# Kernel optimization log

Measured on AMD Instinct MI355X. Metric: run time of the kernel, lower is better.

Reference implementation:

```python
import jax, jax.numpy as jnp
import numpy as np

N, E, IN, H, C = 20000, 320000, 512, 4, 64
HC = H * C
EPS_BN = 1e-5


def setup_inputs() -> dict:
    key = jax.random.key(0)
    ks = jax.random.split(key, 12)
    p = lambda k, shape, s=0.05: jax.random.normal(k, shape, dtype=jnp.float32) * s
    z = lambda n: jnp.zeros((n,), jnp.float32)
    o = lambda n: jnp.ones((n,), jnp.float32)
    return {
        "x": jax.random.normal(ks[0], (N, IN), dtype=jnp.float32),
        "edge_index": jax.random.randint(ks[1], (2, E), 0, N),
        "Wl0": p(ks[2], (IN, HC)), "Wr0": p(ks[3], (IN, HC)),
        "att0": p(ks[4], (H, C)), "b0": z(HC),
        "g0": o(HC), "be0": z(HC), "m0": z(HC), "v0": o(HC),
        "Wl1": p(ks[5], (HC, HC)), "Wr1": p(ks[6], (HC, HC)),
        "att1": p(ks[7], (H, C)), "b1": z(HC),
        "g1": o(HC), "be1": z(HC), "m1": z(HC), "v1": o(HC),
        "Wl2": p(ks[8], (HC, 2)), "Wr2": p(ks[9], (HC, 2)),
        "att2": p(ks[10], (1, 2)), "b2": z(2),
    }


def gatv2_conv(x, Wl, Wr, att, b, ei, concat):
    # GATv2: e_ij = att . LeakyReLU(Wl x_j + Wr x_i); softmax over in-edges of i
    n = x.shape[0]
    h, c = att.shape
    xl = (x @ Wl).reshape(n, h, c)  # source/message transform
    xr = (x @ Wr).reshape(n, h, c)  # target transform
    src, dst = ei[0], ei[1]
    m = xl[src] + xr[dst]                                   # [E,H,C] edge gather
    e = jnp.sum(jax.nn.leaky_relu(m, 0.2) * att, axis=-1)   # [E,H]
    emax = jax.ops.segment_max(e, dst, num_segments=n)      # segment softmax
    emax = jnp.where(jnp.isfinite(emax), emax, 0.0)
    ex = jnp.exp(e - emax[dst])
    denom = jax.ops.segment_sum(ex, dst, num_segments=n)
    alpha = ex / (denom[dst] + 1e-16)                       # [E,H]
    out = jax.ops.segment_sum(alpha[:, :, None] * xl[src], dst, num_segments=n)
    out = out.reshape(n, h * c) if concat else out.mean(axis=1)
    return out + b


def bn_eval(x, g, be, m, v):
    return (x - m) * (g * jax.lax.rsqrt(v + EPS_BN)) + be


def reference(x, edge_index, Wl0, Wr0, att0, b0, g0, be0, m0, v0,
              Wl1, Wr1, att1, b1, g1, be1, m1, v1, Wl2, Wr2, att2, b2):
    loops = jnp.arange(N)
    ei = jnp.concatenate([edge_index, jnp.stack([loops, loops])], axis=1)
    h = gatv2_conv(x, Wl0, Wr0, att0, b0, ei, True)
    h = jax.nn.elu(bn_eval(h, g0, be0, m0, v0))
    h = gatv2_conv(h, Wl1, Wr1, att1, b1, ei, True)
    h = jax.nn.elu(bn_eval(h, g1, be1, m1, v1))
    out = gatv2_conv(h, Wl2, Wr2, att2, b2, ei, False)
    return jax.nn.log_softmax(out, axis=1)
```

## Files before the change

kernel.cpp:

```cpp
#include <hip/hip_runtime.h>
#include <math.h>

#define NN 20000
#define MP 20096
#define EE 320000
#define ET (EE + NN)
#define HC 256
#define EPS_BN 1e-5f

#define PB_CX 5000
#define PB_W0 1024
#define PB_W1 512
#define PB_HIST 1329
#define PB_TOTAL (PB_CX + PB_W0 + PB_W1 + PB_HIST)

typedef __bf16 bf16x8 __attribute__((ext_vector_type(8)));
typedef float f32x4 __attribute__((ext_vector_type(4)));

__device__ __forceinline__ float4 ld4(const float* p) { return *reinterpret_cast<const float4*>(p); }
__device__ __forceinline__ float lrelu(float x) { return fmaxf(x, 0.f) + 0.2f * fminf(x, 0.f); }

__device__ __forceinline__ unsigned short f2b(float f) {
  unsigned int u = __float_as_uint(f);
  u = (u + 0x7fffu + ((u >> 16) & 1u)) >> 16;
  return (unsigned short)u;
}
__device__ __forceinline__ float b2f(unsigned short u) {
  return __uint_as_float(((unsigned int)u) << 16);
}

__device__ __forceinline__ void gld_lds16(const void* g, void* l) {
  __builtin_amdgcn_global_load_lds(
      (const __attribute__((address_space(1))) unsigned int*)g,
      (__attribute__((address_space(3))) unsigned int*)(unsigned int)(unsigned long long)l,
      16, 0, 0);
}

__global__ __launch_bounds__(256) void prep_kernel(const float* __restrict__ x,
                                                   unsigned short* __restrict__ xb,
                                                   const float* __restrict__ Wl0,
                                                   const float* __restrict__ Wr0,
                                                   unsigned short* __restrict__ Wf0,
                                                   const float* __restrict__ Wl1,
                                                   const float* __restrict__ Wr1,
                                                   unsigned short* __restrict__ Wf1,
                                                   const int* __restrict__ ei,
                                                   int* __restrict__ counts) {
  const int b = blockIdx.x;
  const int tid = threadIdx.x;
  if (b < PB_CX) {
    int i = (b * 256 + tid) * 8;
    float4 v0 = ld4(&x[i]);
    float4 v1 = ld4(&x[i + 4]);
    ushort4 o0, o1;
    o0.x = f2b(v0.x); o0.y = f2b(v0.y); o0.z = f2b(v0.z); o0.w = f2b(v0.w);
    o1.x = f2b(v1.x); o1.y = f2b(v1.y); o1.z = f2b(v1.z); o1.w = f2b(v1.w);
    *reinterpret_cast<ushort4*>(&xb[i]) = o0;
    *reinterpret_cast<ushort4*>(&xb[i + 4]) = o1;
  } else if (b < PB_CX + PB_W0) {
    int idx = (b - PB_CX) * 256 + tid;
    int n = idx >> 9, k = idx & 511;
    float v = (n < 256) ? Wl0[(size_t)k * 256 + n] : Wr0[(size_t)k * 256 + (n - 256)];
    Wf0[idx] = f2b(v);
  } else if (b < PB_CX + PB_W0 + PB_W1) {
    int idx = (b - PB_CX - PB_W0) * 256 + tid;
    int n = idx >> 8, k = idx & 255;
    float v = (n < 256) ? Wl1[(size_t)k * 256 + n] : Wr1[(size_t)k * 256 + (n - 256)];
    Wf1[idx] = f2b(v);
  } else {
    int e = (b - PB_CX - PB_W0 - PB_W1) * 256 + tid;
    if (e < ET) {
      int d = (e < EE) ? ei[EE + e] : (e - EE);
      atomicAdd(&counts[d], 1);
    }
  }
}

__global__ __launch_bounds__(256) void gemm_mfma(const unsigned short* __restrict__ A,
                                                 const unsigned short* __restrict__ Bt,
                                                 unsigned short* __restrict__ xlb,
                                                 float* __restrict__ xrf,
                                                 int M, int K) {
  __shared__ unsigned short As[128 * 32];
  __shared__ unsigned short Bs[128 * 32];
  const int wave = threadIdx.x >> 6;
  const int lane = threadIdx.x & 63;
  const int am = lane & 15;
  const int aq = lane >> 4;
  const int wr = (wave >> 1) * 64;
  const int wc = (wave & 1) * 64;
  const int row0 = blockIdx.y * 128;
  const int col0 = blockIdx.x * 128;

  f32x4 acc[4][4] = {};

  for (int kk = 0; kk < K; kk += 32) {
    __syncthreads();
#pragma unroll
    for (int c = 0; c < 2; ++c) {
      int seg = wave * 128 + c * 64 + lane;
      int r = seg >> 2, ks = (seg & 3) * 8;
      gld_lds16(A + (size_t)(row0 + r) * K + kk + ks, &As[(wave * 128 + c * 64) * 8]);
      gld_lds16(Bt + (size_t)(col0 + r) * K + kk + ks, &Bs[(wave * 128 + c * 64) * 8]);
    }
    __syncthreads();

    bf16x8 af[4], bfr[4];
#pragma unroll
    for (int i = 0; i < 4; ++i)
      af[i] = *reinterpret_cast<const bf16x8*>(&As[(wr + i * 16 + am) * 32 + aq * 8]);
#pragma unroll
    for (int j = 0; j < 4; ++j)
      bfr[j] = *reinterpret_cast<const bf16x8*>(&Bs[(wc + j * 16 + am) * 32 + aq * 8]);
#pragma unroll
    for (int i = 0; i < 4; ++i)
#pragma unroll
      for (int j = 0; j < 4; ++j)
        acc[i][j] = __builtin_amdgcn_mfma_f32_16x16x32_bf16(af[i], bfr[j], acc[i][j], 0, 0, 0);
  }

#pragma unroll
  for (int i = 0; i < 4; ++i) {
#pragma unroll
    for (int j = 0; j < 4; ++j) {
      int gcol = col0 + wc + j * 16 + am;
#pragma unroll
      for (int rr = 0; rr < 4; ++rr) {
        int grow = row0 + wr + i * 16 + aq * 4 + rr;
        if (grow < M) {
          float v = acc[i][j][rr];
          if (gcol < 256) xlb[(size_t)grow * 256 + gcol] = f2b(v);
          else            xrf[(size_t)grow * 256 + (gcol - 256)] = v;
        }
      }
    }
  }
}

__global__ __launch_bounds__(1024) void scan_kernel(int* __restrict__ cursor,
                                                    int* __restrict__ offsets) {
  __shared__ int wsum[16];
  const int tid = threadIdx.x;
  const int lane = tid & 63, wv = tid >> 6;
  const int base = tid * 20;
  int vals[20];
  int s = 0;
  if (tid < 1000) {
#pragma unroll
    for (int j = 0; j < 20; ++j) { vals[j] = cursor[base + j]; s += vals[j]; }
  }
  int ssum = s;
#pragma unroll
  for (int off = 1; off < 64; off <<= 1) {
    int t = __shfl_up(ssum, off);
    if (lane >= off) ssum += t;
  }
  if (lane == 63) wsum[wv] = ssum;
  __syncthreads();
  if (wv == 0) {
    int w = (lane < 16) ? wsum[lane] : 0;
#pragma unroll
    for (int off = 1; off < 16; off <<= 1) {
      int t = __shfl_up(w, off);
      if (lane >= off) w += t;
    }
    if (lane < 16) wsum[lane] = w;
  }
  __syncthreads();
  int excl = ssum - s + (wv > 0 ? wsum[wv - 1] : 0);
  if (tid < 1000) {
    int run = excl;
#pragma unroll
    for (int j = 0; j < 20; ++j) { offsets[base + j] = run; cursor[base + j] = run; run += vals[j]; }
  }
  if (tid == 1023) offsets[NN] = wsum[15];
}

__global__ __launch_bounds__(256) void scatter_kernel(const int* __restrict__ ei,
                                                      int* __restrict__ cursor,
                                                      int* __restrict__ srcs) {
  int e = blockIdx.x * blockDim.x + threadIdx.x;
  if (e >= ET) return;
  int s, d;
  if (e < EE) { s = ei[e]; d = ei[EE + e]; } else { s = d = e - EE; }
  int pos = atomicAdd(&cursor[d], 1);
  srcs[pos] = s;
}

__global__ __launch_bounds__(256) void gat_layer(const unsigned short* __restrict__ xlb,
                                                 const float* __restrict__ xrf,
                                                 const float* __restrict__ att,
                                                 const float* __restrict__ bias,
                                                 const float* __restrict__ gam,
                                                 const float* __restrict__ bet,
                                                 const float* __restrict__ mean,
                                                 const float* __restrict__ var,
                                                 const int* __restrict__ offsets,
                                                 const int* __restrict__ srcs,
                                                 unsigned short* __restrict__ hb) {
  const int wave = threadIdx.x >> 6;
  const int lane = threadIdx.x & 63;
  const int node = blockIdx.x * 4 + wave;
  if (node >= NN) return;

  const float4 xr4 = ld4(&xrf[(size_t)node * HC + lane * 4]);
  const float4 a4 = ld4(&att[lane * 4]);
  const int beg = offsets[node];
  const int deg = offsets[node + 1] - beg;

  float lA = 0.f, lB = 0.f;
  float4 OA = make_float4(0.f, 0.f, 0.f, 0.f);
  float4 OB = make_float4(0.f, 0.f, 0.f, 0.f);

  for (int base = 0; base < deg; base += 64) {
    const int chunk = min(64, deg - base);
    const int s_reg = srcs[beg + base + min(lane, chunk - 1)];
    const int nb = (chunk + 3) >> 2;

    ushort4 buf0[4], buf1[4], buf2[4];

#define ISSUE(r, buf)                                                              \
    {                                                                              \
      _Pragma("unroll")                                                            \
      for (int j = 0; j < 4; ++j) {                                                \
        int idx = (r) * 4 + j;                                                     \
        int sv = __shfl(s_reg, idx < chunk ? idx : 0);                             \
        buf[j] = *reinterpret_cast<const ushort4*>(&xlb[(size_t)sv * HC + lane * 4]); \
      }                                                                            \
    }

#define COMPUTE(r, buf)                                                            \
    {                                                                              \
      float e[4], xv[4][4];                                                        \
      _Pragma("unroll")                                                            \
      for (int j = 0; j < 4; ++j) {                                                \
        xv[j][0] = b2f(buf[j].x); xv[j][1] = b2f(buf[j].y);                        \
        xv[j][2] = b2f(buf[j].z); xv[j][3] = b2f(buf[j].w);                        \
        e[j] = lrelu(xv[j][0] + xr4.x) * a4.x + lrelu(xv[j][1] + xr4.y) * a4.y +   \
               lrelu(xv[j][2] + xr4.z) * a4.z + lrelu(xv[j][3] + xr4.w) * a4.w;    \
      }                                                                            \
      _Pragma("unroll")                                                            \
      for (int off = 1; off < 16; off <<= 1) {                                     \
        e[0] += __shfl_xor(e[0], off); e[1] += __shfl_xor(e[1], off);              \
        e[2] += __shfl_xor(e[2], off); e[3] += __shfl_xor(e[3], off);              \
      }                                                                            \
      float p0 = __expf(e[0]), p1 = __expf(e[1]);                                  \
      float p2 = __expf(e[2]), p3 = __expf(e[3]);                                  \
      if ((r) * 4 + 0 >= chunk) p0 = 0.f;                                          \
      if ((r) * 4 + 1 >= chunk) p1 = 0.f;                                          \
      if ((r) * 4 + 2 >= chunk) p2 = 0.f;                                          \
      if ((r) * 4 + 3 >= chunk) p3 = 0.f;                                          \
      lA += p0; lB += p1; lA += p2; lB += p3;                                      \
      OA.x += p0 * xv[0][0]; OA.y += p0 * xv[0][1];                                \
      OA.z += p0 * xv[0][2]; OA.w += p0 * xv[0][3];                                \
      OB.x += p1 * xv[1][0]; OB.y += p1 * xv[1][1];                                \
      OB.z += p1 * xv[1][2]; OB.w += p1 * xv[1][3];                                \
      OA.x += p2 * xv[2][0]; OA.y += p2 * xv[2][1];                                \
      OA.z += p2 * xv[2][2]; OA.w += p2 * xv[2][3];                                \
      OB.x += p3 * xv[3][0]; OB.y += p3 * xv[3][1];                                \
      OB.z += p3 * xv[3][2]; OB.w += p3 * xv[3][3];                                \
    }

    ISSUE(0, buf0);
    ISSUE(1, buf1);
    ISSUE(2, buf2);
    int r = 0;
    while (r < nb) {
      COMPUTE(r, buf0); if (r + 3 < nb) ISSUE(r + 3, buf0); ++r;
      if (r >= nb) break;
      COMPUTE(r, buf1); if (r + 3 < nb) ISSUE(r + 3, buf1); ++r;
      if (r >= nb) break;
      COMPUTE(r, buf2); if (r + 3 < nb) ISSUE(r + 3, buf2); ++r;
    }
#undef ISSUE
#undef COMPUTE
  }

  float inv = 1.f / (lA + lB);
  float4 O = make_float4(OA.x + OB.x, OA.y + OB.y, OA.z + OB.z, OA.w + OB.w);

  float4 b4 = ld4(&bias[lane * 4]);
  float4 g4 = ld4(&gam[lane * 4]);
  float4 e4 = ld4(&bet[lane * 4]);
  float4 m4 = ld4(&mean[lane * 4]);
  float4 v4 = ld4(&var[lane * 4]);
  float y0 = O.x * inv + b4.x, y1 = O.y * inv + b4.y;
  float y2 = O.z * inv + b4.z, y3 = O.w * inv + b4.w;
  float z0 = (y0 - m4.x) * (g4.x * rsqrtf(v4.x + EPS_BN)) + e4.x;
  float z1 = (y1 - m4.y) * (g4.y * rsqrtf(v4.y + EPS_BN)) + e4.y;
  float z2 = (y2 - m4.z) * (g4.z * rsqrtf(v4.z + EPS_BN)) + e4.z;
  float z3 = (y3 - m4.w) * (g4.w * rsqrtf(v4.w + EPS_BN)) + e4.w;
  ushort4 r4o;
  r4o.x = f2b(z0 > 0.f ? z0 : expm1f(z0));
  r4o.y = f2b(z1 > 0.f ? z1 : expm1f(z1));
  r4o.z = f2b(z2 > 0.f ? z2 : expm1f(z2));
  r4o.w = f2b(z3 > 0.f ? z3 : expm1f(z3));
  *reinterpret_cast<ushort4*>(&hb[(size_t)node * HC + lane * 4]) = r4o;
}

__global__ __launch_bounds__(256) void lin2_kernel(const unsigned short* __restrict__ hb,
                                                   const float* __restrict__ Wl,
                                                   const float* __restrict__ Wr,
                                                   float* __restrict__ xl2,
                                                   float* __restrict__ xr2) {
  const int wave = threadIdx.x >> 6;
  const int lane = threadIdx.x & 63;
  const int node = blockIdx.x * 4 + wave;
  if (node >= NN) return;
  ushort4 h4 = *reinterpret_cast<const ushort4*>(&hb[(size_t)node * HC + lane * 4]);
  float hv[4] = {b2f(h4.x), b2f(h4.y), b2f(h4.z), b2f(h4.w)};
  float l0 = 0.f, l1 = 0.f, r0 = 0.f, r1 = 0.f;
#pragma unroll
  for (int j = 0; j < 4; ++j) {
    int row = lane * 4 + j;
    l0 += hv[j] * Wl[row * 2 + 0];
    l1 += hv[j] * Wl[row * 2 + 1];
    r0 += hv[j] * Wr[row * 2 + 0];
    r1 += hv[j] * Wr[row * 2 + 1];
  }
#pragma unroll
  for (int off = 1; off < 64; off <<= 1) {
    l0 += __shfl_xor(l0, off);
    l1 += __shfl_xor(l1, off);
    r0 += __shfl_xor(r0, off);
    r1 += __shfl_xor(r1, off);
  }
  if (lane == 0) {
    xl2[node * 2 + 0] = l0; xl2[node * 2 + 1] = l1;
    xr2[node * 2 + 0] = r0; xr2[node * 2 + 1] = r1;
  }
}

__global__ __launch_bounds__(256) void gat2_out_kernel(const float* __restrict__ xl2,
                                                       const float* __restrict__ xr2,
                                                       const float* __restrict__ att2,
                                                       const float* __restrict__ b2,
                                                       const int* __restrict__ offsets,
                                                       const int* __restrict__ srcs,
                                                       float* __restrict__ out) {
  const int wave = threadIdx.x >> 6;
  const int lane = threadIdx.x & 63;
  const int node = blockIdx.x * 4 + wave;
  if (node >= NN) return;
  const float a0 = att2[0], a1 = att2[1];
  const float xr0 = xr2[node * 2 + 0], xr1 = xr2[node * 2 + 1];
  const int beg = offsets[node], end = offsets[node + 1];

  float l = 0.f, o0 = 0.f, o1 = 0.f;
  for (int i = beg + lane; i < end; i += 64) {
    int s = srcs[i];
    float x0 = xl2[s * 2 + 0], x1 = xl2[s * 2 + 1];
    float e = lrelu(x0 + xr0) * a0 + lrelu(x1 + xr1) * a1;
    float p = __expf(e);
    l += p;
    o0 += p * x0;
    o1 += p * x1;
  }
#pragma unroll
  for (int off = 1; off < 64; off <<= 1) {
    l += __shfl_xor(l, off);
    o0 += __shfl_xor(o0, off);
    o1 += __shfl_xor(o1, off);
  }
  if (lane == 0) {
    float inv = 1.f / l;
    float t0 = o0 * inv + b2[0];
    float t1 = o1 * inv + b2[1];
    float mx = fmaxf(t0, t1);
    float ls = mx + logf(__expf(t0 - mx) + __expf(t1 - mx));
    out[node * 2 + 0] = t0 - ls;
    out[node * 2 + 1] = t1 - ls;
  }
}

extern "C" void kernel_launch(void* const* d_in, const int* in_sizes, int n_in,
                              void* d_out, int out_size, void* d_ws, size_t ws_size,
                              hipStream_t stream) {
  const float* x    = (const float*)d_in[0];
  const int*   ei   = (const int*)d_in[1];
  const float* Wl0  = (const float*)d_in[2];
  const float* Wr0  = (const float*)d_in[3];
  const float* att0 = (const float*)d_in[4];
  const float* b0   = (const float*)d_in[5];
  const float* g0   = (const float*)d_in[6];
  const float* be0  = (const float*)d_in[7];
  const float* m0   = (const float*)d_in[8];
  const float* v0   = (const float*)d_in[9];
  const float* Wl1  = (const float*)d_in[10];
  const float* Wr1  = (const float*)d_in[11];
  const float* att1 = (const float*)d_in[12];
  const float* b1   = (const float*)d_in[13];
  const float* g1   = (const float*)d_in[14];
  const float* be1  = (const float*)d_in[15];
  const float* m1   = (const float*)d_in[16];
  const float* v1   = (const float*)d_in[17];
  const float* Wl2  = (const float*)d_in[18];
  const float* Wr2  = (const float*)d_in[19];
  const float* att2 = (const float*)d_in[20];
  const float* b2   = (const float*)d_in[21];

  float* xrf = (float*)d_ws;
  unsigned short* xlb = (unsigned short*)(xrf + (size_t)NN * 256);
  unsigned short* hb  = xlb + (size_t)NN * 256;
  unsigned short* xb  = hb + (size_t)MP * 256;
  unsigned short* Wf0 = xb + (size_t)MP * 512;
  unsigned short* Wf1 = Wf0 + 512 * 512;
  float* xl2 = (float*)(Wf1 + 512 * 256);
  float* xr2 = xl2 + 2 * NN;
  int* offsets = (int*)(xr2 + 2 * NN);
  int* cursor  = offsets + (NN + 1);
  int* srcs    = cursor + NN;

  hipMemsetAsync(cursor, 0, NN * sizeof(int), stream);
  prep_kernel<<<PB_TOTAL, 256, 0, stream>>>(x, xb, Wl0, Wr0, Wf0, Wl1, Wr1, Wf1, ei, cursor);
  scan_kernel<<<1, 1024, 0, stream>>>(cursor, offsets);
  scatter_kernel<<<(ET + 255) / 256, 256, 0, stream>>>(ei, cursor, srcs);

  dim3 gemm_grid(4, MP / 128);
  gemm_mfma<<<gemm_grid, 256, 0, stream>>>(xb, Wf0, xlb, xrf, NN, 512);
  gat_layer<<<NN / 4, 256, 0, stream>>>(xlb, xrf, att0, b0, g0, be0, m0, v0, offsets, srcs, hb);
  gemm_mfma<<<gemm_grid, 256, 0, stream>>>(hb, Wf1, xlb, xrf, NN, 256);
  gat_layer<<<NN / 4, 256, 0, stream>>>(xlb, xrf, att1, b1, g1, be1, m1, v1, offsets, srcs, hb);
  lin2_kernel<<<NN / 4, 256, 0, stream>>>(hb, Wl2, Wr2, xl2, xr2);
  gat2_out_kernel<<<NN / 4, 256, 0, stream>>>(xl2, xr2, att2, b2, offsets, srcs, (float*)d_out);
}
```

Before: 310.4 us.

## Fuse layer-2 linear projection into GAT layer1 and simplify edge gather loop

The layer-1 GAT aggregation kernel now computes the final 256->2 projections (Wl2, Wr2) directly from its fp32 post-ELU values. This removes the lin2 kernel launch and the bf16 hidden-state write and read-back. The edge loop is also rewritten: instead of a 64-edge chunked, shuffle-broadcast, triple-buffered pipeline, it loads sources directly in unrolled groups of 8, then 4, then single edges. The new loop gives up explicit software prefetch across groups and relies on unrolled independent loads for latency hiding.

```diff
diff --git a/kernel.cpp b/kernel.cpp
--- a/kernel.cpp
+++ b/kernel.cpp
@@ -187,17 +187,104 @@
   srcs[pos] = s;
 }
 
-__global__ __launch_bounds__(256) void gat_layer(const unsigned short* __restrict__ xlb,
-                                                 const float* __restrict__ xrf,
-                                                 const float* __restrict__ att,
-                                                 const float* __restrict__ bias,
-                                                 const float* __restrict__ gam,
-                                                 const float* __restrict__ bet,
-                                                 const float* __restrict__ mean,
-                                                 const float* __restrict__ var,
-                                                 const int* __restrict__ offsets,
-                                                 const int* __restrict__ srcs,
-                                                 unsigned short* __restrict__ hb) {
+#define GAT_ACCUM_BODY                                                              \
+  float lacc[4] = {0.f, 0.f, 0.f, 0.f};                                             \
+  float4 Ob[4];                                                                     \
+  Ob[0] = make_float4(0.f, 0.f, 0.f, 0.f); Ob[1] = Ob[0];                           \
+  Ob[2] = Ob[0]; Ob[3] = Ob[0];                                                     \
+  int i = beg;                                                                      \
+  for (; i + 7 < end; i += 8) {                                                     \
+    ushort4 u[8];                                                                   \
+    _Pragma("unroll")                                                               \
+    for (int j = 0; j < 8; ++j) {                                                   \
+      int s = srcs[i + j];                                                          \
+      u[j] = *reinterpret_cast<const ushort4*>(&xlb[(size_t)s * HC + lane * 4]);    \
+    }                                                                               \
+    float e[8]; float4 xv[8];                                                       \
+    _Pragma("unroll")                                                               \
+    for (int j = 0; j < 8; ++j) {                                                   \
+      xv[j] = make_float4(b2f(u[j].x), b2f(u[j].y), b2f(u[j].z), b2f(u[j].w));      \
+      e[j] = lrelu(xv[j].x + xr4.x) * a4.x + lrelu(xv[j].y + xr4.y) * a4.y +        \
+             lrelu(xv[j].z + xr4.z) * a4.z + lrelu(xv[j].w + xr4.w) * a4.w;         \
+    }                                                                               \
+    _Pragma("unroll")                                                               \
+    for (int off = 1; off < 16; off <<= 1) {                                        \
+      _Pragma("unroll")                                                             \
+      for (int j = 0; j < 8; ++j) e[j] += __shfl_xor(e[j], off);                    \
+    }                                                                               \
+    _Pragma("unroll")                                                               \
+    for (int j = 0; j < 8; ++j) {                                                   \
+      float p = __expf(e[j]);                                                       \
+      lacc[j & 3] += p;                                                             \
+      Ob[j & 3].x += p * xv[j].x; Ob[j & 3].y += p * xv[j].y;                       \
+      Ob[j & 3].z += p * xv[j].z; Ob[j & 3].w += p * xv[j].w;                       \
+    }                                                                               \
+  }                                                                                 \
+  for (; i + 3 < end; i += 4) {                                                     \
+    ushort4 u[4];                                                                   \
+    _Pragma("unroll")                                                               \
+    for (int j = 0; j < 4; ++j) {                                                   \
+      int s = srcs[i + j];                                                          \
+      u[j] = *reinterpret_cast<const ushort4*>(&xlb[(size_t)s * HC + lane * 4]);    \
+    }                                                                               \
+    float e[4]; float4 xv[4];                                                       \
+    _Pragma("unroll")                                                               \
+    for (int j = 0; j < 4; ++j) {                                                   \
+      xv[j] = make_float4(b2f(u[j].x), b2f(u[j].y), b2f(u[j].z), b2f(u[j].w));      \
+      e[j] = lrelu(xv[j].x + xr4.x) * a4.x + lrelu(xv[j].y + xr4.y) * a4.y +        \
+             lrelu(xv[j].z + xr4.z) * a4.z + lrelu(xv[j].w + xr4.w) * a4.w;         \
+    }                                                                               \
+    _Pragma("unroll")                                                               \
+    for (int off = 1; off < 16; off <<= 1) {                                        \
+      _Pragma("unroll")                                                             \
+      for (int j = 0; j < 4; ++j) e[j] += __shfl_xor(e[j], off);                    \
+    }                                                                               \
+    _Pragma("unroll")                                                               \
+    for (int j = 0; j < 4; ++j) {                                                   \
+      float p = __expf(e[j]);                                                       \
+      lacc[j] += p;                                                                 \
+      Ob[j].x += p * xv[j].x; Ob[j].y += p * xv[j].y;                               \
+      Ob[j].z += p * xv[j].z; Ob[j].w += p * xv[j].w;                               \
+    }                                                                               \
+  }                                                                                 \
+  for (; i < end; ++i) {                                                            \
+    int s = srcs[i];                                                                \
+    ushort4 u = *reinterpret_cast<const ushort4*>(&xlb[(size_t)s * HC + lane * 4]); \
+    float4 xv = make_float4(b2f(u.x), b2f(u.y), b2f(u.z), b2f(u.w));                \
+    float e = lrelu(xv.x + xr4.x) * a4.x + lrelu(xv.y + xr4.y) * a4.y +             \
+              lrelu(xv.z + xr4.z) * a4.z + lrelu(xv.w + xr4.w) * a4.w;              \
+    _Pragma("unroll")                                                               \
+    for (int off = 1; off < 16; off <<= 1) e += __shfl_xor(e, off);                 \
+    float p = __expf(e);                                                            \
+    lacc[0] += p;                                                                   \
+    Ob[0].x += p * xv.x; Ob[0].y += p * xv.y;                                       \
+    Ob[0].z += p * xv.z; Ob[0].w += p * xv.w;                                       \
+  }                                                                                 \
+  float inv = 1.f / (lacc[0] + lacc[1] + lacc[2] + lacc[3]);                        \
+  float y0 = (Ob[0].x + Ob[1].x + Ob[2].x + Ob[3].x) * inv + b4.x;                  \
+  float y1 = (Ob[0].y + Ob[1].y + Ob[2].y + Ob[3].y) * inv + b4.y;                  \
+  float y2 = (Ob[0].z + Ob[1].z + Ob[2].z + Ob[3].z) * inv + b4.z;                  \
+  float y3 = (Ob[0].w + Ob[1].w + Ob[2].w + Ob[3].w) * inv + b4.w;                  \
+  float z0 = (y0 - m4.x) * (g4.x * rsqrtf(v4.x + EPS_BN)) + e4.x;                   \
+  float z1 = (y1 - m4.y) * (g4.y * rsqrtf(v4.y + EPS_BN)) + e4.y;                   \
+  float z2 = (y2 - m4.z) * (g4.z * rsqrtf(v4.z + EPS_BN)) + e4.z;                   \
+  float z3 = (y3 - m4.w) * (g4.w * rsqrtf(v4.w + EPS_BN)) + e4.w;                   \
+  z0 = (z0 > 0.f) ? z0 : expm1f(z0);                                                \
+  z1 = (z1 > 0.f) ? z1 : expm1f(z1);                                                \
+  z2 = (z2 > 0.f) ? z2 : expm1f(z2);                                                \
+  z3 = (z3 > 0.f) ? z3 : expm1f(z3);
+
+__global__ __launch_bounds__(256) void gat_layer0(const unsigned short* __restrict__ xlb,
+                                                  const float* __restrict__ xrf,
+                                                  const float* __restrict__ att,
+                                                  const float* __restrict__ bias,
+                                                  const float* __restrict__ gam,
+                                                  const float* __restrict__ bet,
+                                                  const float* __restrict__ mean,
+                                                  const float* __restrict__ var,
+                                                  const int* __restrict__ offsets,
+                                                  const int* __restrict__ srcs,
+                                                  unsigned short* __restrict__ hb) {
   const int wave = threadIdx.x >> 6;
   const int lane = threadIdx.x & 63;
   const int node = blockIdx.x * 4 + wave;
@@ -205,129 +292,75 @@
 
   const float4 xr4 = ld4(&xrf[(size_t)node * HC + lane * 4]);
   const float4 a4 = ld4(&att[lane * 4]);
+  const float4 b4 = ld4(&bias[lane * 4]);
+  const float4 g4 = ld4(&gam[lane * 4]);
+  const float4 e4 = ld4(&bet[lane * 4]);
+  const float4 m4 = ld4(&mean[lane * 4]);
+  const float4 v4 = ld4(&var[lane * 4]);
   const int beg = offsets[node];
-  const int deg = offsets[node + 1] - beg;
-
-  float lA = 0.f, lB = 0.f;
-  float4 OA = make_float4(0.f, 0.f, 0.f, 0.f);
-  float4 OB = make_float4(0.f, 0.f, 0.f, 0.f);
-
-  for (int base = 0; base < deg; base += 64) {
-    const int chunk = min(64, deg - base);
-    const int s_reg = srcs[beg + base + min(lane, chunk - 1)];
-    const int nb = (chunk + 3) >> 2;
-
-    ushort4 buf0[4], buf1[4], buf2[4];
-
-#define ISSUE(r, buf)                                                              \
-    {                                                                              \
-      _Pragma("unroll")                                                            \
-      for (int j = 0; j < 4; ++j) {                                                \
-        int idx = (r) * 4 + j;                                                     \
-        int sv = __shfl(s_reg, idx < chunk ? idx : 0);                             \
-        buf[j] = *reinterpret_cast<const ushort4*>(&xlb[(size_t)sv * HC + lane * 4]); \
-      }                                                                            \
-    }
-
-#define COMPUTE(r, buf)                                                            \
-    {                                                                              \
-      float e[4], xv[4][4];                                                        \
-      _Pragma("unroll")                                                            \
-      for (int j = 0; j < 4; ++j) {                                                \
-        xv[j][0] = b2f(buf[j].x); xv[j][1] = b2f(buf[j].y);                        \
-        xv[j][2] = b2f(buf[j].z); xv[j][3] = b2f(buf[j].w);                        \
-        e[j] = lrelu(xv[j][0] + xr4.x) * a4.x + lrelu(xv[j][1] + xr4.y) * a4.y +   \
-               lrelu(xv[j][2] + xr4.z) * a4.z + lrelu(xv[j][3] + xr4.w) * a4.w;    \
-      }                                                                            \
-      _Pragma("unroll")                                                            \
-      for (int off = 1; off < 16; off <<= 1) {                                     \
-        e[0] += __shfl_xor(e[0], off); e[1] += __shfl_xor(e[1], off);              \
-        e[2] += __shfl_xor(e[2], off); e[3] += __shfl_xor(e[3], off);              \
-      }                                                                            \
-      float p0 = __expf(e[0]), p1 = __expf(e[1]);                                  \
-      float p2 = __expf(e[2]), p3 = __expf(e[3]);                                  \
-      if ((r) * 4 + 0 >= chunk) p0 = 0.f;                                          \
-      if ((r) * 4 + 1 >= chunk) p1 = 0.f;                                          \
-      if ((r) * 4 + 2 >= chunk) p2 = 0.f;                                          \
-      if ((r) * 4 + 3 >= chunk) p3 = 0.f;                                          \
-      lA += p0; lB += p1; lA += p2; lB += p3;                                      \
-      OA.x += p0 * xv[0][0]; OA.y += p0 * xv[0][1];                                \
-      OA.z += p0 * xv[0][2]; OA.w += p0 * xv[0][3];                                \
-      OB.x += p1 * xv[1][0]; OB.y += p1 * xv[1][1];                                \
-      OB.z += p1 * xv[1][2]; OB.w += p1 * xv[1][3];                                \
-      OA.x += p2 * xv[2][0]; OA.y += p2 * xv[2][1];                                \
-      OA.z += p2 * xv[2][2]; OA.w += p2 * xv[2][3];                                \
-      OB.x += p3 * xv[3][0]; OB.y += p3 * xv[3][1];                                \
-      OB.z += p3 * xv[3][2]; OB.w += p3 * xv[3][3];                                \
-    }
-
-    ISSUE(0, buf0);
-    ISSUE(1, buf1);
-    ISSUE(2, buf2);
-    int r = 0;
-    while (r < nb) {
-      COMPUTE(r, buf0); if (r + 3 < nb) ISSUE(r + 3, buf0); ++r;
-      if (r >= nb) break;
-      COMPUTE(r, buf1); if (r + 3 < nb) ISSUE(r + 3, buf1); ++r;
-      if (r >= nb) break;
-      COMPUTE(r, buf2); if (r + 3 < nb) ISSUE(r + 3, buf2); ++r;
-    }
-#undef ISSUE
-#undef COMPUTE
-  }
-
-  float inv = 1.f / (lA + lB);
-  float4 O = make_float4(OA.x + OB.x, OA.y + OB.y, OA.z + OB.z, OA.w + OB.w);
-
-  float4 b4 = ld4(&bias[lane * 4]);
-  float4 g4 = ld4(&gam[lane * 4]);
-  float4 e4 = ld4(&bet[lane * 4]);
-  float4 m4 = ld4(&mean[lane * 4]);
-  float4 v4 = ld4(&var[lane * 4]);
-  float y0 = O.x * inv + b4.x, y1 = O.y * inv + b4.y;
-  float y2 = O.z * inv + b4.z, y3 = O.w * inv + b4.w;
-  float z0 = (y0 - m4.x) * (g4.x * rsqrtf(v4.x + EPS_BN)) + e4.x;
-  float z1 = (y1 - m4.y) * (g4.y * rsqrtf(v4.y + EPS_BN)) + e4.y;
-  float z2 = (y2 - m4.z) * (g4.z * rsqrtf(v4.z + EPS_BN)) + e4.z;
-  float z3 = (y3 - m4.w) * (g4.w * rsqrtf(v4.w + EPS_BN)) + e4.w;
-  ushort4 r4o;
-  r4o.x = f2b(z0 > 0.f ? z0 : expm1f(z0));
-  r4o.y = f2b(z1 > 0.f ? z1 : expm1f(z1));
-  r4o.z = f2b(z2 > 0.f ? z2 : expm1f(z2));
-  r4o.w = f2b(z3 > 0.f ? z3 : expm1f(z3));
-  *reinterpret_cast<ushort4*>(&hb[(size_t)node * HC + lane * 4]) = r4o;
-}
-
-__global__ __launch_bounds__(256) void lin2_kernel(const unsigned short* __restrict__ hb,
-                                                   const float* __restrict__ Wl,
-                                                   const float* __restrict__ Wr,
-                                                   float* __restrict__ xl2,
-                                                   float* __restrict__ xr2) {
+  const int end = offsets[node + 1];
+
+  GAT_ACCUM_BODY
+
+  ushort4 r;
+  r.x = f2b(z0); r.y = f2b(z1); r.z = f2b(z2); r.w = f2b(z3);
+  *reinterpret_cast<ushort4*>(&hb[(size_t)node * HC + lane * 4]) = r;
+}
+
+__global__ __launch_bounds__(256) void gat_layer1(const unsigned short* __restrict__ xlb,
+                                                  const float* __restrict__ xrf,
+                                                  const float* __restrict__ att,
+                                                  const float* __restrict__ bias,
+                                                  const float* __restrict__ gam,
+                                                  const float* __restrict__ bet,
+                                                  const float* __restrict__ mean,
+                                                  const float* __restrict__ var,
+                                                  const int* __restrict__ offsets,
+                                                  const int* __restrict__ srcs,
+                                                  const float* __restrict__ Wl2,
+                                                  const float* __restrict__ Wr2,
+                                                  float* __restrict__ xl2,
+                                                  float* __restrict__ xr2) {
   const int wave = threadIdx.x >> 6;
   const int lane = threadIdx.x & 63;
   const int node = blockIdx.x * 4 + wave;
   if (node >= NN) return;
-  ushort4 h4 = *reinterpret_cast<const ushort4*>(&hb[(size_t)node * HC + lane * 4]);
-  float hv[4] = {b2f(h4.x), b2f(h4.y), b2f(h4.z), b2f(h4.w)};
-  float l0 = 0.f, l1 = 0.f, r0 = 0.f, r1 = 0.f;
-#pragma unroll
-  for (int j = 0; j < 4; ++j) {
-    int row = lane * 4 + j;
-    l0 += hv[j] * Wl[row * 2 + 0];
-    l1 += hv[j] * Wl[row * 2 + 1];
-    r0 += hv[j] * Wr[row * 2 + 0];
-    r1 += hv[j] * Wr[row * 2 + 1];
-  }
+
+  const float4 xr4 = ld4(&xrf[(size_t)node * HC + lane * 4]);
+  const float4 a4 = ld4(&att[lane * 4]);
+  const float4 b4 = ld4(&bias[lane * 4]);
+  const float4 g4 = ld4(&gam[lane * 4]);
+  const float4 e4 = ld4(&bet[lane * 4]);
+  const float4 m4 = ld4(&mean[lane * 4]);
+  const float4 v4 = ld4(&var[lane * 4]);
+  const int row = lane * 4;
+  const float wl00 = Wl2[(row + 0) * 2], wl01 = Wl2[(row + 0) * 2 + 1];
+  const float wl10 = Wl2[(row + 1) * 2], wl11 = Wl2[(row + 1) * 2 + 1];
+  const float wl20 = Wl2[(row + 2) * 2], wl21 = Wl2[(row + 2) * 2 + 1];
+  const float wl30 = Wl2[(row + 3) * 2], wl31 = Wl2[(row + 3) * 2 + 1];
+  const float wr00 = Wr2[(row + 0) * 2], wr01 = Wr2[(row + 0) * 2 + 1];
+  const float wr10 = Wr2[(row + 1) * 2], wr11 = Wr2[(row + 1) * 2 + 1];
+  const float wr20 = Wr2[(row + 2) * 2], wr21 = Wr2[(row + 2) * 2 + 1];
+  const float wr30 = Wr2[(row + 3) * 2], wr31 = Wr2[(row + 3) * 2 + 1];
+  const int beg = offsets[node];
+  const int end = offsets[node + 1];
+
+  GAT_ACCUM_BODY
+
+  float pl0 = z0 * wl00 + z1 * wl10 + z2 * wl20 + z3 * wl30;
+  float pl1 = z0 * wl01 + z1 * wl11 + z2 * wl21 + z3 * wl31;
+  float pr0 = z0 * wr00 + z1 * wr10 + z2 * wr20 + z3 * wr30;
+  float pr1 = z0 * wr01 + z1 * wr11 + z2 * wr21 + z3 * wr31;
 #pragma unroll
   for (int off = 1; off < 64; off <<= 1) {
-    l0 += __shfl_xor(l0, off);
-    l1 += __shfl_xor(l1, off);
-    r0 += __shfl_xor(r0, off);
-    r1 += __shfl_xor(r1, off);
+    pl0 += __shfl_xor(pl0, off);
+    pl1 += __shfl_xor(pl1, off);
+    pr0 += __shfl_xor(pr0, off);
+    pr1 += __shfl_xor(pr1, off);
   }
   if (lane == 0) {
-    xl2[node * 2 + 0] = l0; xl2[node * 2 + 1] = l1;
-    xr2[node * 2 + 0] = r0; xr2[node * 2 + 1] = r1;
+    xl2[node * 2 + 0] = pl0; xl2[node * 2 + 1] = pl1;
+    xr2[node * 2 + 0] = pr0; xr2[node * 2 + 1] = pr1;
   }
 }
 
@@ -418,9 +451,9 @@
 
   dim3 gemm_grid(4, MP / 128);
   gemm_mfma<<<gemm_grid, 256, 0, stream>>>(xb, Wf0, xlb, xrf, NN, 512);
-  gat_layer<<<NN / 4, 256, 0, stream>>>(xlb, xrf, att0, b0, g0, be0, m0, v0, offsets, srcs, hb);
+  gat_layer0<<<NN / 4, 256, 0, stream>>>(xlb, xrf, att0, b0, g0, be0, m0, v0, offsets, srcs, hb);
   gemm_mfma<<<gemm_grid, 256, 0, stream>>>(hb, Wf1, xlb, xrf, NN, 256);
-  gat_layer<<<NN / 4, 256, 0, stream>>>(xlb, xrf, att1, b1, g1, be1, m1, v1, offsets, srcs, hb);
-  lin2_kernel<<<NN / 4, 256, 0, stream>>>(hb, Wl2, Wr2, xl2, xr2);
+  gat_layer1<<<NN / 4, 256, 0, stream>>>(xlb, xrf, att1, b1, g1, be1, m1, v1, offsets, srcs,
+                                         Wl2, Wr2, xl2, xr2);
   gat2_out_kernel<<<NN / 4, 256, 0, stream>>>(xl2, xr2, att2, b2, offsets, srcs, (float*)d_out);
 }
```

After: 321.4 us. 3.5% more time.
